# Kernel tuning notes

Measured on AMD Instinct MI355X. Metric: run time of the kernel, lower is better.

Reference implementation:

```python
import jax, jax.numpy as jnp
import numpy as np

SIGMA = 1.0
TOP_K = 4

def setup_inputs() -> dict:
    key = jax.random.key(0)
    k1, k2, k3, k4 = jax.random.split(key, 4)
    B, N, IN_DIM, OUT_DIM, P = 2, 4096, 128, 128, 3
    x = jax.random.normal(k1, (B, N, IN_DIM), dtype=jnp.float32)
    pos = jax.random.normal(k2, (B, N, P), dtype=jnp.float32)
    # Linear(in_dim, out_dim): W [in_dim, out_dim], b [out_dim]
    lim = 1.0 / np.sqrt(IN_DIM)
    W = jax.random.uniform(k3, (IN_DIM, OUT_DIM), minval=-lim, maxval=lim, dtype=jnp.float32)
    b = jax.random.uniform(k4, (OUT_DIM,), minval=-lim, maxval=lim, dtype=jnp.float32)
    return {"x": x, "pos": pos, "W": W, "b": b}

def reference(x, pos, W, b):
    B, N, _ = x.shape
    # pairwise distances [B, N, N]
    pos_diff = pos[:, :, None, :] - pos[:, None, :, :]
    dist = jnp.sqrt(jnp.sum(pos_diff ** 2, axis=-1) + 1e-8)
    adj = jnp.exp(-dist ** 2 / (2.0 * SIGMA ** 2))
    # top-k mask along last dim
    _, indices = jax.lax.top_k(adj, TOP_K)  # [B, N, k]
    b_idx = jnp.arange(B)[:, None, None]
    n_idx = jnp.arange(N)[None, :, None]
    mask = jnp.zeros_like(adj).at[b_idx, n_idx, indices].set(1.0)
    adj = adj * mask
    adj = adj / (jnp.sum(adj, axis=-1, keepdims=True) + 1e-8)
    # weighted aggregation + linear
    out = jnp.einsum('bnm,bmd->bnd', adj, x)
    return out @ W + b
```

## Files before the change

kernel.cpp:

```cpp
#include <hip/hip_runtime.h>
#include <hip/hip_bf16.h>

#define NPTS 4096
#define NROWS 8192
#define DIM 128

typedef __attribute__((ext_vector_type(8))) short bf16x8;
typedef __attribute__((ext_vector_type(4))) float f32x4;

__global__ __launch_bounds__(256) void prep(const float* __restrict__ pos,
                                            const float* __restrict__ W,
                                            float4* __restrict__ pos4,
                                            __hip_bfloat16* __restrict__ Wt) {
    int t = blockIdx.x * 256 + threadIdx.x;
    if (t < NROWS) {
        const float* p = pos + (size_t)t * 3;
        pos4[t] = make_float4(p[0], p[1], p[2], 0.f);
    } else if (t < NROWS + DIM * DIM) {
        int i = t - NROWS;
        int n = i >> 7, k = i & 127;
        Wt[i] = __float2bfloat16(W[k * DIM + n]);
    }
}

__global__ __launch_bounds__(256) void xw_mfma(const float* __restrict__ x,
                                               const __hip_bfloat16* __restrict__ Wt,
                                               __hip_bfloat16* __restrict__ xWb) {
    int wave = threadIdx.x >> 6;
    int lane = threadIdx.x & 63;
    int tile = blockIdx.x * 4 + wave;
    int m0 = (tile >> 3) << 4;
    int n0 = (tile & 7) << 4;
    int r = lane & 15;
    int kg = lane >> 4;
    const float* xr = x + (size_t)(m0 + r) * DIM + kg * 8;
    const __hip_bfloat16* br = Wt + (size_t)(n0 + r) * DIM + kg * 8;
    f32x4 acc = {0.f, 0.f, 0.f, 0.f};
#pragma unroll
    for (int kb = 0; kb < 4; ++kb) {
        float4 a0 = *(const float4*)(xr + kb * 32);
        float4 a1 = *(const float4*)(xr + kb * 32 + 4);
        bf16x8 af;
        union { __hip_bfloat16 h; short s; } u;
        u.h = __float2bfloat16(a0.x); af[0] = u.s;
        u.h = __float2bfloat16(a0.y); af[1] = u.s;
        u.h = __float2bfloat16(a0.z); af[2] = u.s;
        u.h = __float2bfloat16(a0.w); af[3] = u.s;
        u.h = __float2bfloat16(a1.x); af[4] = u.s;
        u.h = __float2bfloat16(a1.y); af[5] = u.s;
        u.h = __float2bfloat16(a1.z); af[6] = u.s;
        u.h = __float2bfloat16(a1.w); af[7] = u.s;
        bf16x8 bfr = *(const bf16x8*)(br + kb * 32);
        acc = __builtin_amdgcn_mfma_f32_16x16x32_bf16(af, bfr, acc, 0, 0, 0);
    }
    int col = n0 + r;
    int rbase = m0 + (kg << 2);
#pragma unroll
    for (int reg = 0; reg < 4; ++reg)
        xWb[(size_t)(rbase + reg) * DIM + col] = __float2bfloat16(acc[reg]);
}

__device__ __forceinline__ double mkkey(float d2, int j) {
    return __longlong_as_double(__double_as_longlong((double)d2) |
                                (unsigned long long)(unsigned)j);
}

__device__ __forceinline__ void kins(double& k0, double& k1, double& k2,
                                     double& k3, double s) {
    double c = fmax(k0, s); k0 = fmin(k0, s);
    double t = fmax(k1, c); k1 = fmin(k1, c); c = t;
    t = fmax(k2, c);        k2 = fmin(k2, c); c = t;
    k3 = fmin(k3, c);
}

__device__ __forceinline__ void kmerge(double& a0, double& a1, double& a2,
                                       double& a3, double b0, double b1,
                                       double b2, double b3) {
    double m0 = fmin(a0, b3), m1 = fmin(a1, b2);
    double m2 = fmin(a2, b1), m3 = fmin(a3, b0);
    double t0 = fmin(m0, m2), t2 = fmax(m0, m2);
    double t1 = fmin(m1, m3), t3 = fmax(m1, m3);
    a0 = fmin(t0, t1); a1 = fmax(t0, t1);
    a2 = fmin(t2, t3); a3 = fmax(t2, t3);
}

__global__ __launch_bounds__(256) void topk_agg(const float4* __restrict__ pos4,
                                                const __hip_bfloat16* __restrict__ xWb,
                                                const float* __restrict__ bias,
                                                float* __restrict__ out) {
    int lane = threadIdx.x & 63;
    int wave = threadIdx.x >> 6;
    int group = wave >> 1;
    int half = wave & 1;
    int rowbase = blockIdx.x * 4 + group * 2;
    int batch = rowbase >> 12;
    int ibase = rowbase & (NPTS - 1);
    const float4* pb = pos4 + (size_t)batch * NPTS;

    float4 q0 = pb[ibase], q1 = pb[ibase + 1];
    const double INF = __builtin_inf();
    double a0 = INF, a1 = INF, a2 = INF, a3 = INF;
    double b0 = INF, b1 = INF, b2 = INF, b3 = INF;

    int jbase = (half << 11) + lane;
#pragma unroll 4
    for (int t = 0; t < 32; ++t) {
        int j = jbase + (t << 6);
        float4 p = pb[j];
        float dx = q0.x - p.x, dy = q0.y - p.y, dz = q0.z - p.z;
        float d2 = fmaf(dx, dx, fmaf(dy, dy, dz * dz));
        kins(a0, a1, a2, a3, mkkey(d2, j));
        dx = q1.x - p.x; dy = q1.y - p.y; dz = q1.z - p.z;
        d2 = fmaf(dx, dx, fmaf(dy, dy, dz * dz));
        kins(b0, b1, b2, b3, mkkey(d2, j));
    }

#pragma unroll
    for (int off = 1; off < 64; off <<= 1) {
        double p0 = __shfl_xor(a0, off), p1 = __shfl_xor(a1, off);
        double p2 = __shfl_xor(a2, off), p3 = __shfl_xor(a3, off);
        kmerge(a0, a1, a2, a3, p0, p1, p2, p3);
        p0 = __shfl_xor(b0, off); p1 = __shfl_xor(b1, off);
        p2 = __shfl_xor(b2, off); p3 = __shfl_xor(b3, off);
        kmerge(b0, b1, b2, b3, p0, p1, p2, p3);
    }

    __shared__ double lds[2][2][2][4];
    if (lane == 0) {
        lds[group][half][0][0] = a0; lds[group][half][0][1] = a1;
        lds[group][half][0][2] = a2; lds[group][half][0][3] = a3;
        lds[group][half][1][0] = b0; lds[group][half][1][1] = b1;
        lds[group][half][1][2] = b2; lds[group][half][1][3] = b3;
    }
    __syncthreads();
    if (half) return;

    kmerge(a0, a1, a2, a3, lds[group][1][0][0], lds[group][1][0][1],
                           lds[group][1][0][2], lds[group][1][0][3]);
    kmerge(b0, b1, b2, b3, lds[group][1][1][0], lds[group][1][1][1],
                           lds[group][1][1][2], lds[group][1][1][3]);

    int c = lane << 1;
    float2 bb = *(const float2*)(bias + c);
    const unsigned short* xu = (const unsigned short*)xWb;
    size_t bbase = ((size_t)batch * NPTS) << 7;
#pragma unroll
    for (int k = 0; k < 2; ++k) {
        double k0 = k ? b0 : a0, k1 = k ? b1 : a1;
        double k2 = k ? b2 : a2, k3 = k ? b3 : a3;
        unsigned i0 = (unsigned)__double_as_longlong(k0) & 0xFFFu;
        unsigned i1 = (unsigned)__double_as_longlong(k1) & 0xFFFu;
        unsigned i2 = (unsigned)__double_as_longlong(k2) & 0xFFFu;
        unsigned i3 = (unsigned)__double_as_longlong(k3) & 0xFFFu;
        float d0 = (float)k0, d1 = (float)k1, d2 = (float)k2, d3 = (float)k3;
        float w0 = __expf(-(d0 + 1e-8f) * 0.5f);
        float w1 = __expf(-(d1 + 1e-8f) * 0.5f);
        float w2 = __expf(-(d2 + 1e-8f) * 0.5f);
        float w3 = __expf(-(d3 + 1e-8f) * 0.5f);
        float inv = 1.0f / (w0 + w1 + w2 + w3 + 1e-8f);
        w0 *= inv; w1 *= inv; w2 *= inv; w3 *= inv;
        ushort2 g0 = *(const ushort2*)(xu + bbase + ((size_t)i0 << 7) + c);
        ushort2 g1 = *(const ushort2*)(xu + bbase + ((size_t)i1 << 7) + c);
        ushort2 g2 = *(const ushort2*)(xu + bbase + ((size_t)i2 << 7) + c);
        ushort2 g3 = *(const ushort2*)(xu + bbase + ((size_t)i3 << 7) + c);
        float ox = bb.x + w0 * __uint_as_float((unsigned)g0.x << 16)
                        + w1 * __uint_as_float((unsigned)g1.x << 16)
                        + w2 * __uint_as_float((unsigned)g2.x << 16)
                        + w3 * __uint_as_float((unsigned)g3.x << 16);
        float oy = bb.y + w0 * __uint_as_float((unsigned)g0.y << 16)
                        + w1 * __uint_as_float((unsigned)g1.y << 16)
                        + w2 * __uint_as_float((unsigned)g2.y << 16)
                        + w3 * __uint_as_float((unsigned)g3.y << 16);
        *(float2*)(out + (((size_t)(rowbase + k)) << 7) + c) = make_float2(ox, oy);
    }
}

extern "C" void kernel_launch(void* const* d_in, const int* in_sizes, int n_in,
                              void* d_out, int out_size, void* d_ws, size_t ws_size,
                              hipStream_t stream) {
    const float* x    = (const float*)d_in[0];
    const float* pos  = (const float*)d_in[1];
    const float* W    = (const float*)d_in[2];
    const float* bias = (const float*)d_in[3];
    float* out = (float*)d_out;

    char* ws = (char*)d_ws;
    __hip_bfloat16* xWb = (__hip_bfloat16*)ws;
    float4* pos4 = (float4*)(ws + (size_t)NROWS * DIM * 2);
    __hip_bfloat16* Wt = (__hip_bfloat16*)(ws + (size_t)NROWS * DIM * 2
                                              + (size_t)NROWS * 16);

    prep<<<(NROWS + DIM * DIM + 255) / 256, 256, 0, stream>>>(pos, W, pos4, Wt);
    xw_mfma<<<(NROWS / 16) * (DIM / 16) / 4, 256, 0, stream>>>(x, Wt, xWb);
    topk_agg<<<NROWS / 4, 256, 0, stream>>>(pos4, xWb, bias, out);
}
```

Measured before the change: 91.36 us.

## Two-pass top-k: float-only threshold scan then ballot-compacted candidate rank

Replaces the double-packed key insertion sort with a first pass that keeps float-only top-4 distances to find the 4th-smallest threshold. A second pass recomputes distances, ballot-compacts candidates at or below the threshold into LDS (capped at 8 per half), and ranks them with shuffles using index-packed double keys for tie-breaking. The goal is to avoid 64-bit min/max ops in the hot loop, at the cost of scanning positions twice, adding syncs, and risking wrong results if more than CAP ties occur.

```diff
diff --git a/kernel.cpp b/kernel.cpp
--- a/kernel.cpp
+++ b/kernel.cpp
@@ -4,6 +4,7 @@
 #define NPTS 4096
 #define NROWS 8192
 #define DIM 128
+#define CAP 8
 
 typedef __attribute__((ext_vector_type(8))) short bf16x8;
 typedef __attribute__((ext_vector_type(4))) float f32x4;
@@ -60,34 +61,33 @@
         xWb[(size_t)(rbase + reg) * DIM + col] = __float2bfloat16(acc[reg]);
 }
 
-__device__ __forceinline__ double mkkey(float d2, int j) {
-    return __longlong_as_double(__double_as_longlong((double)d2) |
-                                (unsigned long long)(unsigned)j);
-}
-
-__device__ __forceinline__ void kins(double& k0, double& k1, double& k2,
-                                     double& k3, double s) {
-    double c = fmax(k0, s); k0 = fmin(k0, s);
-    double t = fmax(k1, c); k1 = fmin(k1, c); c = t;
-    t = fmax(k2, c);        k2 = fmin(k2, c); c = t;
-    k3 = fmin(k3, c);
-}
-
-__device__ __forceinline__ void kmerge(double& a0, double& a1, double& a2,
-                                       double& a3, double b0, double b1,
-                                       double b2, double b3) {
-    double m0 = fmin(a0, b3), m1 = fmin(a1, b2);
-    double m2 = fmin(a2, b1), m3 = fmin(a3, b0);
-    double t0 = fmin(m0, m2), t2 = fmax(m0, m2);
-    double t1 = fmin(m1, m3), t3 = fmax(m1, m3);
-    a0 = fmin(t0, t1); a1 = fmax(t0, t1);
-    a2 = fmin(t2, t3); a3 = fmax(t2, t3);
-}
-
-__global__ __launch_bounds__(256) void topk_agg(const float4* __restrict__ pos4,
-                                                const __hip_bfloat16* __restrict__ xWb,
-                                                const float* __restrict__ bias,
-                                                float* __restrict__ out) {
+__device__ __forceinline__ float dist2(float4 q, float4 p) {
+    float dx = q.x - p.x, dy = q.y - p.y, dz = q.z - p.z;
+    return fmaf(dx, dx, fmaf(dy, dy, dz * dz));
+}
+
+__device__ __forceinline__ void vins(float& k0, float& k1, float& k2, float& k3,
+                                     float s) {
+    float c = fmaxf(k0, s); k0 = fminf(k0, s);
+    float t = fmaxf(k1, c); k1 = fminf(k1, c); c = t;
+    t = fmaxf(k2, c);       k2 = fminf(k2, c); c = t;
+    k3 = fminf(k3, c);
+}
+
+__device__ __forceinline__ void vmerge(float& a0, float& a1, float& a2, float& a3,
+                                       float b0, float b1, float b2, float b3) {
+    float m0 = fminf(a0, b3), m1 = fminf(a1, b2);
+    float m2 = fminf(a2, b1), m3 = fminf(a3, b0);
+    float t0 = fminf(m0, m2), t2 = fmaxf(m0, m2);
+    float t1 = fminf(m1, m3), t3 = fmaxf(m1, m3);
+    a0 = fminf(t0, t1); a1 = fmaxf(t0, t1);
+    a2 = fminf(t2, t3); a3 = fmaxf(t2, t3);
+}
+
+__global__ __launch_bounds__(256, 8) void topk_agg(const float4* __restrict__ pos4,
+                                                   const __hip_bfloat16* __restrict__ xWb,
+                                                   const float* __restrict__ bias,
+                                                   float* __restrict__ out) {
     int lane = threadIdx.x & 63;
     int wave = threadIdx.x >> 6;
     int group = wave >> 1;
@@ -97,48 +97,112 @@
     int ibase = rowbase & (NPTS - 1);
     const float4* pb = pos4 + (size_t)batch * NPTS;
 
+    __shared__ float    vx[2][2][2][4];
+    __shared__ unsigned hidx[2][2][2][CAP];
+    __shared__ float    hdva[2][2][2][CAP];
+    __shared__ unsigned hcnt[2][2][2];
+    __shared__ unsigned fidx[2][2][4];
+    __shared__ float    fdst[2][2][4];
+
     float4 q0 = pb[ibase], q1 = pb[ibase + 1];
-    const double INF = __builtin_inf();
-    double a0 = INF, a1 = INF, a2 = INF, a3 = INF;
-    double b0 = INF, b1 = INF, b2 = INF, b3 = INF;
-
+    const float INF = __int_as_float(0x7f800000);
+    float a0 = INF, a1 = INF, a2 = INF, a3 = INF;
+    float b0 = INF, b1 = INF, b2 = INF, b3 = INF;
     int jbase = (half << 11) + lane;
+
 #pragma unroll 4
+    for (int t = 0; t < 32; ++t) {
+        float4 p = pb[jbase + (t << 6)];
+        vins(a0, a1, a2, a3, dist2(q0, p));
+        vins(b0, b1, b2, b3, dist2(q1, p));
+    }
+#pragma unroll
+    for (int off = 1; off < 64; off <<= 1) {
+        float p0 = __shfl_xor(a0, off), p1 = __shfl_xor(a1, off);
+        float p2 = __shfl_xor(a2, off), p3 = __shfl_xor(a3, off);
+        vmerge(a0, a1, a2, a3, p0, p1, p2, p3);
+        p0 = __shfl_xor(b0, off); p1 = __shfl_xor(b1, off);
+        p2 = __shfl_xor(b2, off); p3 = __shfl_xor(b3, off);
+        vmerge(b0, b1, b2, b3, p0, p1, p2, p3);
+    }
+    if (lane == 0) {
+        vx[group][half][0][0] = a0; vx[group][half][0][1] = a1;
+        vx[group][half][0][2] = a2; vx[group][half][0][3] = a3;
+        vx[group][half][1][0] = b0; vx[group][half][1][1] = b1;
+        vx[group][half][1][2] = b2; vx[group][half][1][3] = b3;
+    }
+    __syncthreads();
+    {
+        int oh = half ^ 1;
+        vmerge(a0, a1, a2, a3, vx[group][oh][0][0], vx[group][oh][0][1],
+                               vx[group][oh][0][2], vx[group][oh][0][3]);
+        vmerge(b0, b1, b2, b3, vx[group][oh][1][0], vx[group][oh][1][1],
+                               vx[group][oh][1][2], vx[group][oh][1][3]);
+    }
+    float t3a = a3, t3b = b3;
+
+    unsigned ca = 0, cb = 0;
+#pragma unroll 2
     for (int t = 0; t < 32; ++t) {
         int j = jbase + (t << 6);
         float4 p = pb[j];
-        float dx = q0.x - p.x, dy = q0.y - p.y, dz = q0.z - p.z;
-        float d2 = fmaf(dx, dx, fmaf(dy, dy, dz * dz));
-        kins(a0, a1, a2, a3, mkkey(d2, j));
-        dx = q1.x - p.x; dy = q1.y - p.y; dz = q1.z - p.z;
-        d2 = fmaf(dx, dx, fmaf(dy, dy, dz * dz));
-        kins(b0, b1, b2, b3, mkkey(d2, j));
-    }
-
-#pragma unroll
-    for (int off = 1; off < 64; off <<= 1) {
-        double p0 = __shfl_xor(a0, off), p1 = __shfl_xor(a1, off);
-        double p2 = __shfl_xor(a2, off), p3 = __shfl_xor(a3, off);
-        kmerge(a0, a1, a2, a3, p0, p1, p2, p3);
-        p0 = __shfl_xor(b0, off); p1 = __shfl_xor(b1, off);
-        p2 = __shfl_xor(b2, off); p3 = __shfl_xor(b3, off);
-        kmerge(b0, b1, b2, b3, p0, p1, p2, p3);
-    }
-
-    __shared__ double lds[2][2][2][4];
+        float da = dist2(q0, p);
+        float db = dist2(q1, p);
+        bool ha = da <= t3a;
+        unsigned long long ma = __ballot(ha);
+        if (ma) {
+            if (ha) {
+                unsigned posn = ca + (unsigned)__popcll(ma & ((1ull << lane) - 1));
+                if (posn < CAP) { hidx[group][0][half][posn] = (unsigned)j;
+                                  hdva[group][0][half][posn] = da; }
+            }
+            ca += (unsigned)__popcll(ma);
+        }
+        bool hb = db <= t3b;
+        unsigned long long mb = __ballot(hb);
+        if (mb) {
+            if (hb) {
+                unsigned posn = cb + (unsigned)__popcll(mb & ((1ull << lane) - 1));
+                if (posn < CAP) { hidx[group][1][half][posn] = (unsigned)j;
+                                  hdva[group][1][half][posn] = db; }
+            }
+            cb += (unsigned)__popcll(mb);
+        }
+    }
     if (lane == 0) {
-        lds[group][half][0][0] = a0; lds[group][half][0][1] = a1;
-        lds[group][half][0][2] = a2; lds[group][half][0][3] = a3;
-        lds[group][half][1][0] = b0; lds[group][half][1][1] = b1;
-        lds[group][half][1][2] = b2; lds[group][half][1][3] = b3;
+        hcnt[group][0][half] = ca < CAP ? ca : CAP;
+        hcnt[group][1][half] = cb < CAP ? cb : CAP;
+    }
+    __syncthreads();
+
+    if (half == 0 && lane < 32) {
+        int r = lane >> 4;
+        int e = lane & 15;
+        unsigned c0 = hcnt[group][r][0], c1 = hcnt[group][r][1];
+        bool valid = (e < CAP) ? ((unsigned)e < c0) : ((unsigned)(e - CAP) < c1);
+        unsigned jj = 0; float dd = 0.f;
+        if (valid) {
+            jj = hidx[group][r][e >= CAP][e & (CAP - 1)];
+            dd = hdva[group][r][e >= CAP][e & (CAP - 1)];
+        }
+        double key = valid
+            ? __longlong_as_double(__double_as_longlong((double)dd) |
+                                   (unsigned long long)jj)
+            : __builtin_inf();
+        int base = lane & 16;
+        int rank = 0;
+#pragma unroll
+        for (int s = 0; s < 16; ++s) {
+            double ks = __shfl(key, base + s);
+            rank += (ks < key) ? 1 : 0;
+        }
+        if (valid && rank < 4) {
+            fidx[group][r][rank] = jj;
+            fdst[group][r][rank] = dd;
+        }
     }
     __syncthreads();
     if (half) return;
-
-    kmerge(a0, a1, a2, a3, lds[group][1][0][0], lds[group][1][0][1],
-                           lds[group][1][0][2], lds[group][1][0][3]);
-    kmerge(b0, b1, b2, b3, lds[group][1][1][0], lds[group][1][1][1],
-                           lds[group][1][1][2], lds[group][1][1][3]);
 
     int c = lane << 1;
     float2 bb = *(const float2*)(bias + c);
@@ -146,13 +210,10 @@
     size_t bbase = ((size_t)batch * NPTS) << 7;
 #pragma unroll
     for (int k = 0; k < 2; ++k) {
-        double k0 = k ? b0 : a0, k1 = k ? b1 : a1;
-        double k2 = k ? b2 : a2, k3 = k ? b3 : a3;
-        unsigned i0 = (unsigned)__double_as_longlong(k0) & 0xFFFu;
-        unsigned i1 = (unsigned)__double_as_longlong(k1) & 0xFFFu;
-        unsigned i2 = (unsigned)__double_as_longlong(k2) & 0xFFFu;
-        unsigned i3 = (unsigned)__double_as_longlong(k3) & 0xFFFu;
-        float d0 = (float)k0, d1 = (float)k1, d2 = (float)k2, d3 = (float)k3;
+        unsigned i0 = fidx[group][k][0], i1 = fidx[group][k][1];
+        unsigned i2 = fidx[group][k][2], i3 = fidx[group][k][3];
+        float d0 = fdst[group][k][0], d1 = fdst[group][k][1];
+        float d2 = fdst[group][k][2], d3 = fdst[group][k][3];
         float w0 = __expf(-(d0 + 1e-8f) * 0.5f);
         float w1 = __expf(-(d1 + 1e-8f) * 0.5f);
         float w2 = __expf(-(d2 + 1e-8f) * 0.5f);
```

Result: slower. 95.24 us (+4.3%).
